# Performance work log

Measured on AMD Instinct MI355X. Metric: run time of the kernel, lower is better.

## Reference

```python
import jax, jax.numpy as jnp
import numpy as np

EPS = 1e-5
C_M, C, C_Z = 256, 32, 128
N_SEQ, N_RES = 256, 1024


def setup_inputs() -> dict:
    key = jax.random.key(0)
    k1, k2, k3 = jax.random.split(key, 3)
    msa = jax.random.normal(k1, (N_SEQ, N_RES, C_M), dtype=jnp.float32)
    norm_w = jnp.ones((C_M,), dtype=jnp.float32)
    norm_b = jnp.zeros((C_M,), dtype=jnp.float32)
    w_ab = jax.random.normal(k2, (C, C_M), dtype=jnp.float32) * (1.0 / np.sqrt(C_M))
    b_ab = jnp.zeros((C,), dtype=jnp.float32)
    w_out = jax.random.normal(k3, (C_Z, C * C), dtype=jnp.float32) * (1.0 / C)
    b_out = jnp.zeros((C_Z,), dtype=jnp.float32)
    return {"msa": msa, "norm_w": norm_w, "norm_b": norm_b,
            "w_ab": w_ab, "b_ab": b_ab, "w_out": w_out, "b_out": b_out}


def reference(msa, norm_w, norm_b, w_ab, b_ab, w_out, b_out):
    # msa: (s, r, c_m) -> (r, s, c_m)
    x = jnp.transpose(msa, (1, 0, 2))
    s = x.shape[1]
    # LayerNorm over c_m
    mu = jnp.mean(x, axis=-1, keepdims=True)
    var = jnp.mean(jnp.square(x - mu), axis=-1, keepdims=True)
    xn = (x - mu) * jax.lax.rsqrt(var + EPS) * norm_w + norm_b
    # a == b: same linear applied twice to same input in the original
    a = jnp.einsum('rsm,cm->rsc', xn, w_ab) + b_ab          # (r, s, c)
    # mean over s of outer product == batched A^T A / s  -> (r, c, c)
    o = jnp.einsum('rsx,rsy->rxy', a, a) / s
    o = o.reshape(o.shape[0], C * C)                        # (r, c*c)
    pre_pair = jnp.einsum('rk,zk->rz', o, w_out) + b_out    # (r, c_z)
    r = pre_pair.shape[0]
    # unsqueeze(1).expand(r, r, c_z)
    pair = jnp.broadcast_to(pre_pair[:, None, :], (r, r, C_Z))
    return pair
```

## Files before the change

### kernel.cpp

```cpp
#include <hip/hip_runtime.h>

#define NSEQ 256
#define NRES 1024
#define CM   256
#define CC   32
#define CZ   128
#define EPS  1e-5f
#define SROW (NRES * CM)
#define XST  68

typedef float f4v __attribute__((ext_vector_type(4)));
typedef __attribute__((ext_vector_type(8))) short short8;
typedef __attribute__((ext_vector_type(4))) float f32x4;
typedef unsigned int u32;

__device__ __forceinline__ float trunc_bf16(float f) {
    return __uint_as_float(__float_as_uint(f) & 0xffff0000u);
}
__device__ __forceinline__ u32 pk_bf16(float a, float b) {
    return (__float_as_uint(b) & 0xffff0000u) | (__float_as_uint(a) >> 16);
}

__global__ void opm_setup(const float* __restrict__ nw,
                          const float* __restrict__ nb,
                          const float* __restrict__ w_ab,
                          const float* __restrict__ b_ab,
                          float* __restrict__ k12,
                          unsigned short* __restrict__ wb_su)
{
    __shared__ float wls[CM * CC];
    const int t = threadIdx.x;
    const float nwm = nw[t];
    #pragma unroll
    for (int c = 0; c < CC; ++c)
        wls[t * CC + c] = nwm * w_ab[c * CM + t];
    __syncthreads();
    if (t < CC) {
        float k1 = 0.f, k2 = 0.f;
        for (int m = 0; m < CM; ++m) {
            k1 += wls[m * CC + t];
            k2 = fmaf(nb[m], w_ab[t * CM + m], k2);
        }
        k12[t]      = k1;
        k12[CC + t] = k2 + b_ab[t];
    }
    for (int e = t; e < 16384; e += 256) {
        const int j     = e & 7;
        const int l     = (e >> 3) & 63;
        const int split = (e >> 9) & 1;
        const int nt    = (e >> 10) & 1;
        const int kk    = e >> 11;
        const int m = (kk << 5) + ((l >> 4) << 3) + j;
        const int c = (nt << 4) + (l & 15);
        const float w  = wls[m * CC + c];
        const float w1 = trunc_bf16(w);
        const float v  = split ? (w - w1) : w;
        wb_su[e] = (unsigned short)(__float_as_uint(v) >> 16);
    }
}

__launch_bounds__(256, 2)
__global__ void opm_compute(const float* __restrict__ msa,
                            const u32*  __restrict__ wb_g,
                            const float* __restrict__ k12,
                            const float* __restrict__ w_out,
                            const float* __restrict__ b_out,
                            float* __restrict__ pre_out)
{
    __shared__ float xp[NSEQ * XST];
    __shared__ float st[512];

    const int tid = threadIdx.x;
    const int r   = blockIdx.x;
    const int w   = tid >> 6;
    const int l   = tid & 63;
    const int lr  = l & 15;
    const int lk  = l >> 4;

    const float* xr = msa + (size_t)tid * SROW + (size_t)r * CM;

    f32x4 acc[4][2];
    #pragma unroll
    for (int mt = 0; mt < 4; ++mt) { acc[mt][0] = (f32x4)0.f; acc[mt][1] = (f32x4)0.f; }
    float psum = 0.f, pssq = 0.f;

    float4 nx[16];
    #pragma unroll
    for (int i = 0; i < 16; ++i)
        nx[i] = *(const float4*)(xr + (i << 2));

    #pragma unroll 1
    for (int c = 0; c < 4; ++c) {
        if (c) __syncthreads();
        #pragma unroll
        for (int i = 0; i < 16; ++i) {
            *(float4*)&xp[tid * XST + (i << 2)] = nx[i];
            psum += (nx[i].x + nx[i].y) + (nx[i].z + nx[i].w);
            pssq  = fmaf(nx[i].x, nx[i].x, fmaf(nx[i].y, nx[i].y,
                    fmaf(nx[i].z, nx[i].z, fmaf(nx[i].w, nx[i].w, pssq))));
        }
        short8 B[2][2][2];
        #pragma unroll
        for (int kk2 = 0; kk2 < 2; ++kk2) {
            const int kk = (c << 1) + kk2;
            #pragma unroll
            for (int nt = 0; nt < 2; ++nt)
                #pragma unroll
                for (int sp = 0; sp < 2; ++sp) {
                    const int fb = ((((kk << 1) + nt) << 1) + sp) * 256 + (l << 2);
                    B[kk2][nt][sp] = __builtin_bit_cast(short8, *(const f4v*)&wb_g[fb]);
                }
        }
        if (c < 3) {
            #pragma unroll
            for (int i = 0; i < 16; ++i)
                nx[i] = *(const float4*)(xr + ((c + 1) << 6) + (i << 2));
        }
        __syncthreads();
        #pragma unroll
        for (int kk2 = 0; kk2 < 2; ++kk2) {
            #pragma unroll
            for (int mt = 0; mt < 4; ++mt) {
                const float* ap = &xp[((w << 6) + (mt << 4) + lr) * XST + (kk2 << 5) + (lk << 3)];
                const float4 pa = *(const float4*)ap;
                const float4 pb = *(const float4*)(ap + 4);
                uint4 u1, u2;
                u1.x = pk_bf16(pa.x, pa.y); u1.y = pk_bf16(pa.z, pa.w);
                u1.z = pk_bf16(pb.x, pb.y); u1.w = pk_bf16(pb.z, pb.w);
                u2.x = pk_bf16(pa.x - trunc_bf16(pa.x), pa.y - trunc_bf16(pa.y));
                u2.y = pk_bf16(pa.z - trunc_bf16(pa.z), pa.w - trunc_bf16(pa.w));
                u2.z = pk_bf16(pb.x - trunc_bf16(pb.x), pb.y - trunc_bf16(pb.y));
                u2.w = pk_bf16(pb.z - trunc_bf16(pb.z), pb.w - trunc_bf16(pb.w));
                const short8 A1 = __builtin_bit_cast(short8, u1);
                const short8 A2 = __builtin_bit_cast(short8, u2);
                acc[mt][0] = __builtin_amdgcn_mfma_f32_16x16x32_bf16(A1, B[kk2][0][0], acc[mt][0], 0, 0, 0);
                acc[mt][1] = __builtin_amdgcn_mfma_f32_16x16x32_bf16(A1, B[kk2][1][0], acc[mt][1], 0, 0, 0);
                acc[mt][0] = __builtin_amdgcn_mfma_f32_16x16x32_bf16(A1, B[kk2][0][1], acc[mt][0], 0, 0, 0);
                acc[mt][1] = __builtin_amdgcn_mfma_f32_16x16x32_bf16(A1, B[kk2][1][1], acc[mt][1], 0, 0, 0);
                acc[mt][0] = __builtin_amdgcn_mfma_f32_16x16x32_bf16(A2, B[kk2][0][0], acc[mt][0], 0, 0, 0);
                acc[mt][1] = __builtin_amdgcn_mfma_f32_16x16x32_bf16(A2, B[kk2][1][0], acc[mt][1], 0, 0, 0);
            }
        }
    }

    {
        const float mu  = psum * (1.f / CM);
        const float var = pssq * (1.f / CM) - mu * mu;
        st[tid]       = mu;
        st[256 + tid] = 1.f / sqrtf(var + EPS);
    }
    __syncthreads();

    float* aB = xp;
    {
        const int cl = lr;
        const float k1_0 = k12[cl],      k1_1 = k12[16 + cl];
        const float k2_0 = k12[CC + cl], k2_1 = k12[CC + 16 + cl];
        #pragma unroll
        for (int mt = 0; mt < 4; ++mt) {
            #pragma unroll
            for (int rg = 0; rg < 4; ++rg) {
                const int s = (w << 6) + (mt << 4) + (lk << 2) + rg;
                const float mu = st[s], rs = st[256 + s];
                const float a0 = fmaf(rs, acc[mt][0][rg] - mu * k1_0, k2_0);
                const float a1 = fmaf(rs, acc[mt][1][rg] - mu * k1_1, k2_1);
                const int sw = s & 7;
                aB[s * CC + (((cl >> 2) ^ sw) << 2) + (cl & 3)]       = a0;
                aB[s * CC + ((((cl >> 2) + 4) ^ sw) << 2) + (cl & 3)] = a1;
            }
        }
    }
    __syncthreads();

    float* scr = xp + 8192;
    const int grp = w;
    const int xs_ = (tid >> 3) & 7;
    const int ys_ = tid & 7;
    float4 pr0 = {0,0,0,0}, pr1 = {0,0,0,0}, pr2 = {0,0,0,0}, pr3 = {0,0,0,0};
    #pragma unroll 4
    for (int si = 0; si < 64; ++si) {
        const int s  = (grp << 6) + si;
        const int sw = s & 7;
        const float4 ax = *(const float4*)&aB[s * CC + ((xs_ ^ sw) << 2)];
        const float4 ay = *(const float4*)&aB[s * CC + ((ys_ ^ sw) << 2)];
        pr0.x = fmaf(ax.x, ay.x, pr0.x); pr0.y = fmaf(ax.x, ay.y, pr0.y);
        pr0.z = fmaf(ax.x, ay.z, pr0.z); pr0.w = fmaf(ax.x, ay.w, pr0.w);
        pr1.x = fmaf(ax.y, ay.x, pr1.x); pr1.y = fmaf(ax.y, ay.y, pr1.y);
        pr1.z = fmaf(ax.y, ay.z, pr1.z); pr1.w = fmaf(ax.y, ay.w, pr1.w);
        pr2.x = fmaf(ax.z, ay.x, pr2.x); pr2.y = fmaf(ax.z, ay.y, pr2.y);
        pr2.z = fmaf(ax.z, ay.z, pr2.z); pr2.w = fmaf(ax.z, ay.w, pr2.w);
        pr3.x = fmaf(ax.w, ay.x, pr3.x); pr3.y = fmaf(ax.w, ay.y, pr3.y);
        pr3.z = fmaf(ax.w, ay.z, pr3.z); pr3.w = fmaf(ax.w, ay.w, pr3.w);
    }
    {
        float* pb = &scr[(grp << 10) + ((xs_ << 2) * CC) + (ys_ << 2)];
        *(float4*)&pb[0 * CC] = pr0;
        *(float4*)&pb[1 * CC] = pr1;
        *(float4*)&pb[2 * CC] = pr2;
        *(float4*)&pb[3 * CC] = pr3;
    }
    __syncthreads();
    {
        const float inv_s = 1.f / NSEQ;
        float4 a4 = *(const float4*)&scr[(tid << 2)];
        const float4 b1 = *(const float4*)&scr[1024 + (tid << 2)];
        const float4 b2 = *(const float4*)&scr[2048 + (tid << 2)];
        const float4 b3 = *(const float4*)&scr[3072 + (tid << 2)];
        a4.x = (a4.x + b1.x + b2.x + b3.x) * inv_s;
        a4.y = (a4.y + b1.y + b2.y + b3.y) * inv_s;
        a4.z = (a4.z + b1.z + b2.z + b3.z) * inv_s;
        a4.w = (a4.w + b1.w + b2.w + b3.w) * inv_s;
        *(float4*)&scr[tid << 2] = a4;
    }
    __syncthreads();

    {
        const int z    = tid & 127;
        const int half = tid >> 7;
        const float* wrow = w_out + (size_t)z * (CC * CC) + half * 512;
        const float* op   = &scr[half * 512];
        float po = 0.f;
        #pragma unroll 8
        for (int k = 0; k < 512; k += 4) {
            const float4 o4 = *(const float4*)&op[k];
            const float4 w4 = *(const float4*)&wrow[k];
            po = fmaf(o4.x, w4.x, fmaf(o4.y, w4.y, fmaf(o4.z, w4.z, fmaf(o4.w, w4.w, po))));
        }
        scr[4096 + (half << 7) + z] = po;
    }
    __syncthreads();
    if (tid < CZ)
        pre_out[(size_t)r * CZ + tid] = scr[4096 + tid] + scr[4096 + CZ + tid] + b_out[tid];
}

__launch_bounds__(256, 8)
__global__ void opm_bcast(const float* __restrict__ pre,
                          float* __restrict__ out)
{
    const int bid = blockIdx.x;
    const int r   = bid >> 3;
    const int jb  = bid & 7;
    const int z4  = threadIdx.x & 31;
    const int jo  = threadIdx.x >> 5;

    const f4v pv = *((const f4v*)(pre + (size_t)r * CZ) + z4);
    f4v* outp = (f4v*)out + ((size_t)r * NRES + (size_t)jb * 128) * (CZ / 4);
    for (int j0 = 0; j0 < 128; j0 += 8)
        __builtin_nontemporal_store(pv, &outp[(size_t)(j0 + jo) * (CZ / 4) + z4]);
}

extern "C" void kernel_launch(void* const* d_in, const int* in_sizes, int n_in,
                              void* d_out, int out_size, void* d_ws, size_t ws_size,
                              hipStream_t stream) {
    const float* msa   = (const float*)d_in[0];
    const float* nw    = (const float*)d_in[1];
    const float* nb    = (const float*)d_in[2];
    const float* w_ab  = (const float*)d_in[3];
    const float* b_ab  = (const float*)d_in[4];
    const float* w_out = (const float*)d_in[5];
    const float* b_out = (const float*)d_in[6];
    float* out = (float*)d_out;

    float* pre = (float*)d_ws;
    float* k12 = pre + (size_t)NRES * CZ;
    unsigned short* wb_su = (unsigned short*)(k12 + 64);

    opm_setup<<<1, 256, 0, stream>>>(nw, nb, w_ab, b_ab, k12, wb_su);
    opm_compute<<<NRES, 256, 0, stream>>>(msa, (const u32*)wb_su, k12, w_out, b_out, pre);
    opm_bcast<<<NRES * 8, 256, 0, stream>>>(pre, out);
}
```

Measured before the change: 791.4 us.

## Split fused kernel into coalesced LayerNorm+projection and separate outer-product kernels

The single per-residue kernel, which read msa with a 1 MB stride per sequence row, is split in two. The first kernel handles 32 contiguous residues of one sequence with fully coalesced loads. It computes LayerNorm statistics and the bf16-split MFMA projection, then writes the 32-channel activations to a workspace in (r, s, c) layout. A second kernel loads each residue's (s, c) activations and performs the outer product and output projection. This adds an extra kernel launch and a 32 MB intermediate round trip through global memory in exchange for better access patterns and higher occupancy.

Result: no change. 792.7 us (+0.2%).

```diff
diff --git a/kernel.cpp b/kernel.cpp
--- a/kernel.cpp
+++ b/kernel.cpp
@@ -6,8 +6,6 @@
 #define CC   32
 #define CZ   128
 #define EPS  1e-5f
-#define SROW (NRES * CM)
-#define XST  68
 
 typedef float f4v __attribute__((ext_vector_type(4)));
 typedef __attribute__((ext_vector_type(8))) short short8;
@@ -59,120 +57,129 @@
     }
 }
 
-__launch_bounds__(256, 2)
-__global__ void opm_compute(const float* __restrict__ msa,
-                            const u32*  __restrict__ wb_g,
-                            const float* __restrict__ k12,
-                            const float* __restrict__ w_out,
-                            const float* __restrict__ b_out,
-                            float* __restrict__ pre_out)
-{
-    __shared__ float xp[NSEQ * XST];
-    __shared__ float st[512];
+__launch_bounds__(256, 4)
+__global__ void opm_lnproj(const float* __restrict__ msa,
+                           const u32*  __restrict__ wb_g,
+                           const float* __restrict__ k12,
+                           float* __restrict__ a_ws)
+{
+    __shared__ float xt[32 * 256];
+    __shared__ float st[64];
 
     const int tid = threadIdx.x;
-    const int r   = blockIdx.x;
+    const int s   = blockIdx.x >> 5;
+    const int r0  = (blockIdx.x & 31) << 5;
     const int w   = tid >> 6;
     const int l   = tid & 63;
     const int lr  = l & 15;
     const int lk  = l >> 4;
-
-    const float* xr = msa + (size_t)tid * SROW + (size_t)r * CM;
-
-    f32x4 acc[4][2];
-    #pragma unroll
-    for (int mt = 0; mt < 4; ++mt) { acc[mt][0] = (f32x4)0.f; acc[mt][1] = (f32x4)0.f; }
+    const int mt  = w & 1;
+    const int nt  = w >> 1;
+
+    const float* xb = msa + ((size_t)s * NRES + r0) * CM;
+
+    float4 pf[8];
+    #pragma unroll
+    for (int j = 0; j < 8; ++j)
+        pf[j] = *(const float4*)(xb + (size_t)(((j << 8) + tid) << 2));
+    #pragma unroll
+    for (int j = 0; j < 8; ++j) {
+        const int row = (j << 2) + w;
+        *(float4*)&xt[(row << 8) + ((l ^ (row & 7)) << 2)] = pf[j];
+    }
+    __syncthreads();
+
+    f32x4 acc = (f32x4)0.f;
     float psum = 0.f, pssq = 0.f;
-
-    float4 nx[16];
-    #pragma unroll
-    for (int i = 0; i < 16; ++i)
-        nx[i] = *(const float4*)(xr + (i << 2));
-
-    #pragma unroll 1
-    for (int c = 0; c < 4; ++c) {
-        if (c) __syncthreads();
-        #pragma unroll
-        for (int i = 0; i < 16; ++i) {
-            *(float4*)&xp[tid * XST + (i << 2)] = nx[i];
-            psum += (nx[i].x + nx[i].y) + (nx[i].z + nx[i].w);
-            pssq  = fmaf(nx[i].x, nx[i].x, fmaf(nx[i].y, nx[i].y,
-                    fmaf(nx[i].z, nx[i].z, fmaf(nx[i].w, nx[i].w, pssq))));
-        }
-        short8 B[2][2][2];
-        #pragma unroll
-        for (int kk2 = 0; kk2 < 2; ++kk2) {
-            const int kk = (c << 1) + kk2;
-            #pragma unroll
-            for (int nt = 0; nt < 2; ++nt)
-                #pragma unroll
-                for (int sp = 0; sp < 2; ++sp) {
-                    const int fb = ((((kk << 1) + nt) << 1) + sp) * 256 + (l << 2);
-                    B[kk2][nt][sp] = __builtin_bit_cast(short8, *(const f4v*)&wb_g[fb]);
-                }
-        }
-        if (c < 3) {
-            #pragma unroll
-            for (int i = 0; i < 16; ++i)
-                nx[i] = *(const float4*)(xr + ((c + 1) << 6) + (i << 2));
-        }
-        __syncthreads();
-        #pragma unroll
-        for (int kk2 = 0; kk2 < 2; ++kk2) {
-            #pragma unroll
-            for (int mt = 0; mt < 4; ++mt) {
-                const float* ap = &xp[((w << 6) + (mt << 4) + lr) * XST + (kk2 << 5) + (lk << 3)];
-                const float4 pa = *(const float4*)ap;
-                const float4 pb = *(const float4*)(ap + 4);
-                uint4 u1, u2;
-                u1.x = pk_bf16(pa.x, pa.y); u1.y = pk_bf16(pa.z, pa.w);
-                u1.z = pk_bf16(pb.x, pb.y); u1.w = pk_bf16(pb.z, pb.w);
-                u2.x = pk_bf16(pa.x - trunc_bf16(pa.x), pa.y - trunc_bf16(pa.y));
-                u2.y = pk_bf16(pa.z - trunc_bf16(pa.z), pa.w - trunc_bf16(pa.w));
-                u2.z = pk_bf16(pb.x - trunc_bf16(pb.x), pb.y - trunc_bf16(pb.y));
-                u2.w = pk_bf16(pb.z - trunc_bf16(pb.z), pb.w - trunc_bf16(pb.w));
-                const short8 A1 = __builtin_bit_cast(short8, u1);
-                const short8 A2 = __builtin_bit_cast(short8, u2);
-                acc[mt][0] = __builtin_amdgcn_mfma_f32_16x16x32_bf16(A1, B[kk2][0][0], acc[mt][0], 0, 0, 0);
-                acc[mt][1] = __builtin_amdgcn_mfma_f32_16x16x32_bf16(A1, B[kk2][1][0], acc[mt][1], 0, 0, 0);
-                acc[mt][0] = __builtin_amdgcn_mfma_f32_16x16x32_bf16(A1, B[kk2][0][1], acc[mt][0], 0, 0, 0);
-                acc[mt][1] = __builtin_amdgcn_mfma_f32_16x16x32_bf16(A1, B[kk2][1][1], acc[mt][1], 0, 0, 0);
-                acc[mt][0] = __builtin_amdgcn_mfma_f32_16x16x32_bf16(A2, B[kk2][0][0], acc[mt][0], 0, 0, 0);
-                acc[mt][1] = __builtin_amdgcn_mfma_f32_16x16x32_bf16(A2, B[kk2][1][0], acc[mt][1], 0, 0, 0);
-            }
-        }
-    }
-
-    {
+    const int arow = ((mt << 4) + lr) << 8;
+    const int sw8  = lr & 7;
+
+    f4v bs0 = *(const f4v*)&wb_g[(((0 + nt) << 1) + 0) * 256 + (l << 2)];
+    f4v bs1 = *(const f4v*)&wb_g[(((0 + nt) << 1) + 1) * 256 + (l << 2)];
+
+    #pragma unroll
+    for (int kk = 0; kk < 8; ++kk) {
+        f4v nb0, nb1;
+        if (kk < 7) {
+            nb0 = *(const f4v*)&wb_g[((((kk + 1) << 1) + nt) << 1) * 256 + (l << 2)];
+            nb1 = *(const f4v*)&wb_g[(((((kk + 1) << 1) + nt) << 1) + 1) * 256 + (l << 2)];
+        }
+        const int m4 = (kk << 3) + (lk << 1);
+        const float4 pa = *(const float4*)&xt[arow + ((m4 ^ sw8) << 2)];
+        const float4 pb = *(const float4*)&xt[arow + (((m4 + 1) ^ sw8) << 2)];
+        psum += ((pa.x + pa.y) + (pa.z + pa.w)) + ((pb.x + pb.y) + (pb.z + pb.w));
+        pssq  = fmaf(pa.x, pa.x, fmaf(pa.y, pa.y, fmaf(pa.z, pa.z, fmaf(pa.w, pa.w, pssq))));
+        pssq  = fmaf(pb.x, pb.x, fmaf(pb.y, pb.y, fmaf(pb.z, pb.z, fmaf(pb.w, pb.w, pssq))));
+        uint4 u1, u2;
+        u1.x = pk_bf16(pa.x, pa.y); u1.y = pk_bf16(pa.z, pa.w);
+        u1.z = pk_bf16(pb.x, pb.y); u1.w = pk_bf16(pb.z, pb.w);
+        u2.x = pk_bf16(pa.x - trunc_bf16(pa.x), pa.y - trunc_bf16(pa.y));
+        u2.y = pk_bf16(pa.z - trunc_bf16(pa.z), pa.w - trunc_bf16(pa.w));
+        u2.z = pk_bf16(pb.x - trunc_bf16(pb.x), pb.y - trunc_bf16(pb.y));
+        u2.w = pk_bf16(pb.z - trunc_bf16(pb.z), pb.w - trunc_bf16(pb.w));
+        const short8 A1 = __builtin_bit_cast(short8, u1);
+        const short8 A2 = __builtin_bit_cast(short8, u2);
+        const short8 B0 = __builtin_bit_cast(short8, bs0);
+        const short8 B1 = __builtin_bit_cast(short8, bs1);
+        acc = __builtin_amdgcn_mfma_f32_16x16x32_bf16(A1, B0, acc, 0, 0, 0);
+        acc = __builtin_amdgcn_mfma_f32_16x16x32_bf16(A1, B1, acc, 0, 0, 0);
+        acc = __builtin_amdgcn_mfma_f32_16x16x32_bf16(A2, B0, acc, 0, 0, 0);
+        if (kk < 7) { bs0 = nb0; bs1 = nb1; }
+    }
+
+    psum += __shfl_xor(psum, 16); psum += __shfl_xor(psum, 32);
+    pssq += __shfl_xor(pssq, 16); pssq += __shfl_xor(pssq, 32);
+    if (nt == 0 && l < 16) {
+        const int R = (mt << 4) + lr;
         const float mu  = psum * (1.f / CM);
         const float var = pssq * (1.f / CM) - mu * mu;
-        st[tid]       = mu;
-        st[256 + tid] = 1.f / sqrtf(var + EPS);
-    }
-    __syncthreads();
-
-    float* aB = xp;
-    {
-        const int cl = lr;
-        const float k1_0 = k12[cl],      k1_1 = k12[16 + cl];
-        const float k2_0 = k12[CC + cl], k2_1 = k12[CC + 16 + cl];
+        st[R]      = mu;
+        st[32 + R] = 1.f / sqrtf(var + EPS);
+    }
+    __syncthreads();
+
+    {
+        const int c  = lr + (nt << 4);
+        const float k1 = k12[c], k2 = k12[CC + c];
         #pragma unroll
-        for (int mt = 0; mt < 4; ++mt) {
-            #pragma unroll
-            for (int rg = 0; rg < 4; ++rg) {
-                const int s = (w << 6) + (mt << 4) + (lk << 2) + rg;
-                const float mu = st[s], rs = st[256 + s];
-                const float a0 = fmaf(rs, acc[mt][0][rg] - mu * k1_0, k2_0);
-                const float a1 = fmaf(rs, acc[mt][1][rg] - mu * k1_1, k2_1);
-                const int sw = s & 7;
-                aB[s * CC + (((cl >> 2) ^ sw) << 2) + (cl & 3)]       = a0;
-                aB[s * CC + ((((cl >> 2) + 4) ^ sw) << 2) + (cl & 3)] = a1;
-            }
-        }
-    }
-    __syncthreads();
-
-    float* scr = xp + 8192;
+        for (int rg = 0; rg < 4; ++rg) {
+            const int R = (mt << 4) + (lk << 2) + rg;
+            const float mu = st[R], rs = st[32 + R];
+            xt[R * CC + c] = fmaf(rs, acc[rg] - mu * k1, k2);
+        }
+    }
+    __syncthreads();
+    {
+        const int row = tid >> 3, c4 = tid & 7;
+        const float4 v = *(const float4*)&xt[row * CC + (c4 << 2)];
+        *(float4*)&a_ws[((size_t)(r0 + row) * NSEQ + s) * CC + (c4 << 2)] = v;
+    }
+}
+
+__launch_bounds__(256, 3)
+__global__ void opm_outer(const float* __restrict__ a_ws,
+                          const float* __restrict__ w_out,
+                          const float* __restrict__ b_out,
+                          float* __restrict__ pre_out)
+{
+    __shared__ float aB[NSEQ * CC];
+    __shared__ float scr[4352];
+
+    const int tid = threadIdx.x;
+    const int r   = blockIdx.x;
+    const int w   = tid >> 6;
+
+    const float* ab = a_ws + (size_t)r * NSEQ * CC;
+    #pragma unroll
+    for (int k = 0; k < 8; ++k) {
+        const int f  = (k << 8) + tid;
+        const int s_ = f >> 3;
+        const int c4 = f & 7;
+        const float4 v = *(const float4*)(ab + ((size_t)f << 2));
+        *(float4*)&aB[s_ * CC + ((c4 ^ (s_ & 7)) << 2)] = v;
+    }
+    __syncthreads();
+
     const int grp = w;
     const int xs_ = (tid >> 3) & 7;
     const int ys_ = tid & 7;
@@ -264,8 +271,10 @@
     float* pre = (float*)d_ws;
     float* k12 = pre + (size_t)NRES * CZ;
     unsigned short* wb_su = (unsigned short*)(k12 + 64);
+    float* a_ws = (float*)(wb_su + 16384);
 
     opm_setup<<<1, 256, 0, stream>>>(nw, nb, w_ab, b_ab, k12, wb_su);
-    opm_compute<<<NRES, 256, 0, stream>>>(msa, (const u32*)wb_su, k12, w_out, b_out, pre);
+    opm_lnproj<<<NSEQ * 32, 256, 0, stream>>>(msa, (const u32*)wb_su, k12, a_ws);
+    opm_outer<<<NRES, 256, 0, stream>>>(a_ws, w_out, b_out, pre);
     opm_bcast<<<NRES * 8, 256, 0, stream>>>(pre, out);
 }
```
